# Kernel optimization log

Measured on AMD Instinct MI355X. Metric: run time of the kernel, lower is better.

## Reference

```python
import jax, jax.numpy as jnp
import numpy as np
from jax import lax

C = 64        # in_channels (== out_channels, kernel is all-ones (C,C,k,k))
KS = 2        # kernel_size
STRIDE = 2


def setup_inputs() -> dict:
    key = jax.random.key(0)
    kx, kc = jax.random.split(key)
    x = jax.random.normal(kx, (32, C, 256, 256), dtype=jnp.float32)
    coef = jax.random.uniform(kc, (C, 1, 1), dtype=jnp.float32)   # torch.rand
    bias = jnp.zeros((C, 1, 1), dtype=jnp.float32)
    return {"x": x, "coef": coef, "bias": bias}


def reference(x, coef, bias):
    # F.conv2d with an all-ones (C,C,k,k) weight: every output channel equals
    # the sum over ALL input channels and the kxk spatial window.
    # Exploit structure: channel-sum -> spatial sum-pool -> broadcast to C -> affine.
    x_csum = jnp.sum(x, axis=1, keepdims=True)  # [B,1,H,W]
    pooled = lax.reduce_window(
        x_csum, jnp.float32(0), lax.add,
        window_dimensions=(1, 1, KS, KS),
        window_strides=(1, 1, STRIDE, STRIDE),
        padding="VALID",
    )  # [B,1,Ho,Wo]
    # broadcast over C via coef/bias of shape (C,1,1)
    return pooled * coef + bias  # [B,C,Ho,Wo]
```

## Files before the change

### kernel.cpp

```cpp
#include <hip/hip_runtime.h>


constexpr int B  = 32;
constexpr int C  = 64;
constexpr int H  = 256;
constexpr int W  = 256;
constexpr int HO = 128;
constexpr int WO = 128;

typedef float floatx4 __attribute__((ext_vector_type(4)));

__global__ __launch_bounds__(256) void subsample_fused_kernel(
    const float* __restrict__ x,
    const float* __restrict__ coef,
    const float* __restrict__ bias,
    float* __restrict__ out)
{
    const int WO2 = WO / 2;
    const int HG  = HO / 2;

    int t   = blockIdx.x * blockDim.x + threadIdx.x;
    int wp  = t % WO2;
    int tmp = t / WO2;
    int hg  = tmp % HG;
    int b   = tmp / HG;
    if (b >= B) return;

    const float* xb = x + (size_t)b * C * H * W + (size_t)(4 * hg) * W + 4 * wp;

    float s00 = 0.f, s01 = 0.f;
    float s10 = 0.f, s11 = 0.f;
    #pragma unroll 4
    for (int c = 0; c < C; ++c) {
        const float* xc = xb + (size_t)c * (H * W);
        floatx4 r0 = __builtin_nontemporal_load(reinterpret_cast<const floatx4*>(xc));
        floatx4 r1 = __builtin_nontemporal_load(reinterpret_cast<const floatx4*>(xc + W));
        floatx4 r2 = __builtin_nontemporal_load(reinterpret_cast<const floatx4*>(xc + 2 * W));
        floatx4 r3 = __builtin_nontemporal_load(reinterpret_cast<const floatx4*>(xc + 3 * W));
        s00 += (r0.x + r0.y) + (r1.x + r1.y);
        s01 += (r0.z + r0.w) + (r1.z + r1.w);
        s10 += (r2.x + r2.y) + (r3.x + r3.y);
        s11 += (r2.z + r2.w) + (r3.z + r3.w);
    }

    float* ob = out + (size_t)b * C * HO * WO + (size_t)(2 * hg) * WO + 2 * wp;
    #pragma unroll 8
    for (int c = 0; c < C; ++c) {
        float k  = coef[c];
        float bs = bias[c];
        float* o0 = ob + (size_t)c * (HO * WO);
        *reinterpret_cast<float2*>(o0)      = make_float2(fmaf(s00, k, bs), fmaf(s01, k, bs));
        *reinterpret_cast<float2*>(o0 + WO) = make_float2(fmaf(s10, k, bs), fmaf(s11, k, bs));
    }
}

extern "C" void kernel_launch(void* const* d_in, const int* in_sizes, int n_in,
                              void* d_out, int out_size, void* d_ws, size_t ws_size,
                              hipStream_t stream) {
    const float* x    = (const float*)d_in[0];
    const float* coef = (const float*)d_in[1];
    const float* bias = (const float*)d_in[2];
    float* out = (float*)d_out;

    const int total = B * (HO / 2) * (WO / 2);
    const int block = 256;
    const int grid  = total / block;

    subsample_fused_kernel<<<grid, block, 0, stream>>>(x, coef, bias, out);
}
```

Measured before the change: 122.4 us.

## Split fused kernel into pool-reduce and coalesced broadcast-affine kernels via workspace

Splits the work into two kernels when a workspace is available. The first reduces channels and pools into a small [B,HO,WO] buffer. The second does a grid-stride broadcast, writing the output in contiguous floatx4 chunks with nontemporal stores. The aim is to replace the scattered float2 stores spread across 64 channel planes with fully coalesced wide writes. The cost is an extra kernel launch and an extra 2 MB round trip through the workspace; if no workspace is provided, the old fused kernel still runs.

```diff
diff --git a/kernel.cpp b/kernel.cpp
--- a/kernel.cpp
+++ b/kernel.cpp
@@ -10,11 +10,9 @@
 
 typedef float floatx4 __attribute__((ext_vector_type(4)));
 
-__global__ __launch_bounds__(256) void subsample_fused_kernel(
+__global__ __launch_bounds__(256) void pool_reduce_kernel(
     const float* __restrict__ x,
-    const float* __restrict__ coef,
-    const float* __restrict__ bias,
-    float* __restrict__ out)
+    float* __restrict__ pooled)
 {
     const int WO2 = WO / 2;
     const int HG  = HO / 2;
@@ -43,11 +41,73 @@
         s11 += (r2.z + r2.w) + (r3.z + r3.w);
     }
 
+    float* pb = pooled + (size_t)b * HO * WO + (size_t)(2 * hg) * WO + 2 * wp;
+    *reinterpret_cast<float2*>(pb)      = make_float2(s00, s01);
+    *reinterpret_cast<float2*>(pb + WO) = make_float2(s10, s11);
+}
+
+__global__ __launch_bounds__(256) void broadcast_affine_kernel(
+    const float* __restrict__ pooled,
+    const float* __restrict__ coef,
+    const float* __restrict__ bias,
+    float* __restrict__ out)
+{
+    const size_t nvec   = (size_t)B * C * HO * (WO / 4);
+    const size_t stride = (size_t)gridDim.x * blockDim.x;
+
+    for (size_t i = blockIdx.x * (size_t)blockDim.x + threadIdx.x;
+         i < nvec; i += stride) {
+        int wq = (int)(i & 31);
+        int ho = (int)((i >> 5) & 127);
+        int c  = (int)((i >> 12) & 63);
+        int b  = (int)(i >> 18);
+
+        floatx4 p = *reinterpret_cast<const floatx4*>(
+            pooled + ((size_t)b * HO + ho) * WO + wq * 4);
+        float k  = coef[c];
+        float bs = bias[c];
+        floatx4 v;
+        v.x = fmaf(p.x, k, bs);
+        v.y = fmaf(p.y, k, bs);
+        v.z = fmaf(p.z, k, bs);
+        v.w = fmaf(p.w, k, bs);
+        __builtin_nontemporal_store(v, reinterpret_cast<floatx4*>(out + i * 4));
+    }
+}
+
+__global__ __launch_bounds__(256) void subsample_fused_kernel(
+    const float* __restrict__ x,
+    const float* __restrict__ coef,
+    const float* __restrict__ bias,
+    float* __restrict__ out)
+{
+    const int WO2 = WO / 2;
+    const int HG  = HO / 2;
+    int t   = blockIdx.x * blockDim.x + threadIdx.x;
+    int wp  = t % WO2;
+    int tmp = t / WO2;
+    int hg  = tmp % HG;
+    int b   = tmp / HG;
+    if (b >= B) return;
+
+    const float* xb = x + (size_t)b * C * H * W + (size_t)(4 * hg) * W + 4 * wp;
+    float s00 = 0.f, s01 = 0.f, s10 = 0.f, s11 = 0.f;
+    #pragma unroll 4
+    for (int c = 0; c < C; ++c) {
+        const float* xc = xb + (size_t)c * (H * W);
+        floatx4 r0 = __builtin_nontemporal_load(reinterpret_cast<const floatx4*>(xc));
+        floatx4 r1 = __builtin_nontemporal_load(reinterpret_cast<const floatx4*>(xc + W));
+        floatx4 r2 = __builtin_nontemporal_load(reinterpret_cast<const floatx4*>(xc + 2 * W));
+        floatx4 r3 = __builtin_nontemporal_load(reinterpret_cast<const floatx4*>(xc + 3 * W));
+        s00 += (r0.x + r0.y) + (r1.x + r1.y);
+        s01 += (r0.z + r0.w) + (r1.z + r1.w);
+        s10 += (r2.x + r2.y) + (r3.x + r3.y);
+        s11 += (r2.z + r2.w) + (r3.z + r3.w);
+    }
     float* ob = out + (size_t)b * C * HO * WO + (size_t)(2 * hg) * WO + 2 * wp;
     #pragma unroll 8
     for (int c = 0; c < C; ++c) {
-        float k  = coef[c];
-        float bs = bias[c];
+        float k = coef[c], bs = bias[c];
         float* o0 = ob + (size_t)c * (HO * WO);
         *reinterpret_cast<float2*>(o0)      = make_float2(fmaf(s00, k, bs), fmaf(s01, k, bs));
         *reinterpret_cast<float2*>(o0 + WO) = make_float2(fmaf(s10, k, bs), fmaf(s11, k, bs));
@@ -62,9 +122,17 @@
     const float* bias = (const float*)d_in[2];
     float* out = (float*)d_out;
 
-    const int total = B * (HO / 2) * (WO / 2);
-    const int block = 256;
-    const int grid  = total / block;
+    const size_t pooled_bytes = (size_t)B * HO * WO * sizeof(float);
 
-    subsample_fused_kernel<<<grid, block, 0, stream>>>(x, coef, bias, out);
+    if (d_ws != nullptr && ws_size >= pooled_bytes) {
+        float* pooled = (float*)d_ws;
+
+        const int total1 = B * (HO / 2) * (WO / 2);
+        pool_reduce_kernel<<<total1 / 256, 256, 0, stream>>>(x, pooled);
+
+        broadcast_affine_kernel<<<2048, 256, 0, stream>>>(pooled, coef, bias, out);
+    } else {
+        const int total = B * (HO / 2) * (WO / 2);
+        subsample_fused_kernel<<<total / 256, 256, 0, stream>>>(x, coef, bias, out);
+    }
 }
```

After: 113.8 us. 7.1% less time.
